# Kernel tuning notes

Hardware: AMD Instinct MI355X
Metric: run time of the kernel (lower is better)

## Reference

```python
import jax, jax.numpy as jnp
import numpy as np

N, T, D, H = 8, 1024, 128, 8

def setup_inputs() -> dict:
    key = jax.random.key(0)
    ks = jax.random.split(key, 6)
    x = jax.random.normal(ks[0], (N, T, D), dtype=jnp.float32)
    attention_mask = jax.random.randint(ks[1], (N, 1, 1, T), 0, 2).astype(jnp.bool_)
    attention_weights = jax.random.uniform(ks[2], (N, H, T, T), dtype=jnp.float32)
    # Linear(dim -> heads*dim) weights, torch convention: W @ x^T + b, W: [H*D, D]
    s = 1.0 / np.sqrt(D)
    Wq = jax.random.normal(ks[3], (H * D, D), dtype=jnp.float32) * s
    Wk = jax.random.normal(ks[4], (H * D, D), dtype=jnp.float32) * s
    Wv = jax.random.normal(ks[5], (H * D, D), dtype=jnp.float32) * s
    bq = jnp.zeros((H * D,), jnp.float32)
    bk = jnp.zeros((H * D,), jnp.float32)
    bv = jnp.zeros((H * D,), jnp.float32)
    return {"x": x, "attention_mask": attention_mask, "attention_weights": attention_weights,
            "Wq": Wq, "bq": bq, "Wk": Wk, "bk": bk, "Wv": Wv, "bv": bv}

def reference(x, attention_mask, attention_weights, Wq, bq, Wk, bk, Wv, bv):
    n, t, d = x.shape
    h = Wq.shape[0] // d
    # projections: [N,T,H*D] -> [N,H,T,D]
    q = (x @ Wq.T + bq).reshape(n, t, h, d).transpose(0, 2, 1, 3)
    k = (x @ Wk.T + bk).reshape(n, t, h, d).transpose(0, 2, 1, 3)
    v = (x @ Wv.T + bv).reshape(n, t, h, d).transpose(0, 2, 1, 3)
    # scores [N,H,T,T]
    att = jnp.einsum('nhtd,nhsd->nhts', q, k) / np.sqrt(d).astype(np.float32)
    att = att * attention_weights
    att = jnp.where(attention_mask, -jnp.inf, att)
    att = jax.nn.softmax(att, axis=-1)
    out = jnp.einsum('nhts,nhsd->nhtd', att, v)
    out = out.transpose(0, 2, 1, 3).reshape(n, t, h * d)
    out_agg = jnp.mean(out, axis=1)
    return out, jax.lax.stop_gradient(out_agg), jax.lax.stop_gradient(att)
```

## Files before the change

kernel.cpp:

```cpp
#include <hip/hip_runtime.h>
#include <hip/hip_bf16.h>
#include <hip/hip_fp16.h>

#define NB 8
#define TT 1024
#define DD 128
#define HH 8

using short8  = __attribute__((ext_vector_type(8))) short;
using floatx4 = __attribute__((ext_vector_type(4))) float;
using half8   = __attribute__((ext_vector_type(8))) _Float16;

__device__ __forceinline__ unsigned short f2bf_u(float f) {
    union { float f; unsigned u; } v; v.f = f;
    return (unsigned short)((v.u + 0x7fffu + ((v.u >> 16) & 1u)) >> 16);
}

__global__ __launch_bounds__(256, 2) void proj_kernel(
    const float* __restrict__ x,
    const float* __restrict__ Wq, const float* __restrict__ bq,
    const float* __restrict__ Wk, const float* __restrict__ bk,
    const float* __restrict__ Wv, const float* __restrict__ bv,
    unsigned short* __restrict__ qb, unsigned short* __restrict__ kb,
    unsigned short* __restrict__ vt)
{
    int b     = blockIdx.x;
    int which = b >> 10;
    int rem   = b & 1023;
    int mblk  = rem >> 3;
    int nblk  = rem & 7;
    int tid   = threadIdx.x;
    int wid   = tid >> 6, lane = tid & 63;
    int l15   = lane & 15, quad = lane >> 4;
    int m0    = mblk * 64 + wid * 16;

    const float* W    = (which == 0) ? Wq : (which == 1) ? Wk : Wv;
    const float* bias = (which == 0) ? bq : (which == 1) ? bk : bv;
    unsigned short* dst = (which == 0) ? qb : (which == 1) ? kb : vt;

    short8 a[4];
    const float* xr = x + (size_t)(m0 + l15) * DD + quad * 8;
    #pragma unroll
    for (int kk = 0; kk < 4; ++kk) {
        const float* p = xr + kk * 32;
        short8 t;
        #pragma unroll
        for (int j = 0; j < 8; ++j) t[j] = (short)f2bf_u(p[j]);
        a[kk] = t;
    }

    floatx4 acc[8];
    #pragma unroll
    for (int ct = 0; ct < 8; ++ct) acc[ct] = (floatx4){0.f, 0.f, 0.f, 0.f};

    for (int ct = 0; ct < 8; ++ct) {
        int c = nblk * 128 + ct * 16 + l15;
        const float* wr = W + (size_t)c * DD + quad * 8;
        #pragma unroll
        for (int kk = 0; kk < 4; ++kk) {
            const float* p = wr + kk * 32;
            short8 bf;
            #pragma unroll
            for (int j = 0; j < 8; ++j) bf[j] = (short)f2bf_u(p[j]);
            acc[ct] = __builtin_amdgcn_mfma_f32_16x16x32_bf16(a[kk], bf, acc[ct], 0, 0, 0);
        }
    }

    #pragma unroll
    for (int ct = 0; ct < 8; ++ct) {
        int c  = nblk * 128 + ct * 16 + l15;
        int h  = c >> 7, dd = c & 127;
        float bsv = bias[c];
        #pragma unroll
        for (int r = 0; r < 4; ++r) {
            int m = m0 + quad * 4 + r;
            int n = m >> 10, t = m & 1023;
            unsigned short v = f2bf_u(acc[ct][r] + bsv);
            size_t idx;
            if (which == 2) idx = ((size_t)(n * HH + h) * DD + dd) * TT + t;
            else            idx = ((size_t)(n * HH + h) * TT + t) * DD + dd;
            dst[idx] = v;
        }
    }
}

#define SSTRIDE 1032

__global__ __launch_bounds__(256, 2) void attn_kernel(
    const unsigned short* __restrict__ qb, const unsigned short* __restrict__ kb,
    const unsigned short* __restrict__ vt,
    const float* __restrict__ wts, const int* __restrict__ mask,
    float* __restrict__ out, float* __restrict__ outagg, float* __restrict__ att)
{
    extern __shared__ char smem[];
    _Float16* S   = (_Float16*)smem;
    float* rowinv = (float*)(smem + 32 * SSTRIDE * 2);

    int b    = blockIdx.x;
    int slot = b & 7, j = b >> 3;
    int tile = j & 31, gq = j >> 5;
    int g    = gq * 8 + slot;
    int n    = g >> 3, h = g & 7;
    int t0   = tile * 32;

    int tid = threadIdx.x;
    int wid = tid >> 6, lane = tid & 63;
    int l15 = lane & 15, quad = lane >> 4;

    const unsigned short* qp = qb + ((size_t)g * TT + t0) * DD;
    const unsigned short* kp = kb + (size_t)g * TT * DD;
    const unsigned short* vp = vt + (size_t)g * DD * TT;
    const float* wp = wts + (size_t)g * TT * TT + (size_t)t0 * TT;
    const int*   mp = mask + n * TT;
    float* attp = att + (size_t)g * TT * TT + (size_t)t0 * TT;

    short8 aq[2][4];
    #pragma unroll
    for (int rt = 0; rt < 2; ++rt)
        #pragma unroll
        for (int kk = 0; kk < 4; ++kk)
            aq[rt][kk] = *(const short8*)(qp + (size_t)(rt * 16 + l15) * DD + kk * 32 + quad * 8);

    const int c0 = wid * 256;
    const float scale = 0.08838834764831845f;
    for (int ct = 0; ct < 16; ++ct) {
        int scol = c0 + ct * 16;
        int mk = mp[scol + l15];
        float w0[4], w1[4];
        #pragma unroll
        for (int r = 0; r < 4; ++r) {
            int row = quad * 4 + r;
            w0[r] = wp[(size_t)row * TT + scol + l15];
            w1[r] = wp[(size_t)(row + 16) * TT + scol + l15];
        }
        floatx4 acc0 = {0.f,0.f,0.f,0.f}, acc1 = {0.f,0.f,0.f,0.f};
        #pragma unroll
        for (int kk = 0; kk < 4; ++kk) {
            short8 bf = *(const short8*)(kp + (size_t)(scol + l15) * DD + kk * 32 + quad * 8);
            acc0 = __builtin_amdgcn_mfma_f32_16x16x32_bf16(aq[0][kk], bf, acc0, 0, 0, 0);
            acc1 = __builtin_amdgcn_mfma_f32_16x16x32_bf16(aq[1][kk], bf, acc1, 0, 0, 0);
        }
        #pragma unroll
        for (int r = 0; r < 4; ++r) {
            int row = quad * 4 + r;
            float s0 = mk ? -65504.f : acc0[r] * scale * w0[r];
            float s1 = mk ? -65504.f : acc1[r] * scale * w1[r];
            S[row * SSTRIDE + scol + l15]        = (_Float16)s0;
            S[(row + 16) * SSTRIDE + scol + l15] = (_Float16)s1;
        }
    }
    __syncthreads();

    int row = tid >> 3;
    int jj  = tid & 7;
    _Float16* Srow = S + row * SSTRIDE + jj * 8;

    float mx = -3.0e38f;
    #pragma unroll 4
    for (int i = 0; i < 16; ++i) {
        half8 hv = *(const half8*)(Srow + i * 64);
        #pragma unroll
        for (int e = 0; e < 8; ++e) mx = fmaxf(mx, (float)hv[e]);
    }
    mx = fmaxf(mx, __shfl_xor(mx, 1));
    mx = fmaxf(mx, __shfl_xor(mx, 2));
    mx = fmaxf(mx, __shfl_xor(mx, 4));

    float sum = 0.f;
    #pragma unroll 4
    for (int i = 0; i < 16; ++i) {
        half8 hv = *(const half8*)(Srow + i * 64);
        #pragma unroll
        for (int e = 0; e < 8; ++e) sum += __expf((float)hv[e] - mx);
    }
    sum += __shfl_xor(sum, 1);
    sum += __shfl_xor(sum, 2);
    sum += __shfl_xor(sum, 4);
    float iv = 1.f / sum;
    if (jj == 0) rowinv[row] = iv;

    float* arow = attp + (size_t)row * TT + jj * 8;
    #pragma unroll 2
    for (int i = 0; i < 16; ++i) {
        half8 hv = *(const half8*)(Srow + i * 64);
        half8 ev;
        floatx4 o0, o1;
        #pragma unroll
        for (int e = 0; e < 8; ++e) {
            float ex = __expf((float)hv[e] - mx);
            ev[e] = __builtin_bit_cast(_Float16, f2bf_u(ex));
            float a = ex * iv;
            if (e < 4) o0[e] = a; else o1[e - 4] = a;
        }
        *(half8*)(Srow + i * 64) = ev;
        *(floatx4*)(arow + i * 64)     = o0;
        *(floatx4*)(arow + i * 64 + 4) = o1;
    }
    __syncthreads();

    int c0p = wid * 32;
    floatx4 o00 = {0.f,0.f,0.f,0.f}, o01 = o00, o10 = o00, o11 = o00;
    #pragma unroll 2
    for (int ks = 0; ks < 32; ++ks) {
        short8 a0 = __builtin_bit_cast(short8,
            *(const half8*)(S + (size_t)l15 * SSTRIDE + ks * 32 + quad * 8));
        short8 a1 = __builtin_bit_cast(short8,
            *(const half8*)(S + (size_t)(16 + l15) * SSTRIDE + ks * 32 + quad * 8));
        short8 b0 = *(const short8*)(vp + (size_t)(c0p + l15) * TT + ks * 32 + quad * 8);
        short8 b1 = *(const short8*)(vp + (size_t)(c0p + 16 + l15) * TT + ks * 32 + quad * 8);
        o00 = __builtin_amdgcn_mfma_f32_16x16x32_bf16(a0, b0, o00, 0, 0, 0);
        o01 = __builtin_amdgcn_mfma_f32_16x16x32_bf16(a0, b1, o01, 0, 0, 0);
        o10 = __builtin_amdgcn_mfma_f32_16x16x32_bf16(a1, b0, o10, 0, 0, 0);
        o11 = __builtin_amdgcn_mfma_f32_16x16x32_bf16(a1, b1, o11, 0, 0, 0);
    }

    #pragma unroll
    for (int ct = 0; ct < 2; ++ct) {
        int col = c0p + ct * 16 + l15;
        float agg = 0.f;
        #pragma unroll
        for (int rt = 0; rt < 2; ++rt) {
            floatx4 oo = (rt == 0) ? (ct == 0 ? o00 : o01) : (ct == 0 ? o10 : o11);
            #pragma unroll
            for (int r = 0; r < 4; ++r) {
                int rw = rt * 16 + quad * 4 + r;
                float val = oo[r] * rowinv[rw];
                out[((size_t)(n * TT + t0 + rw)) * (HH * DD) + h * DD + col] = val;
                agg += val;
            }
        }
        atomicAdd(outagg + n * (HH * DD) + h * DD + col, agg * (1.f / (float)TT));
    }
}

extern "C" void kernel_launch(void* const* d_in, const int* in_sizes, int n_in,
                              void* d_out, int out_size, void* d_ws, size_t ws_size,
                              hipStream_t stream) {
    const float* x    = (const float*)d_in[0];
    const int*   mask = (const int*)d_in[1];
    const float* wts  = (const float*)d_in[2];
    const float* Wq = (const float*)d_in[3];
    const float* bq = (const float*)d_in[4];
    const float* Wk = (const float*)d_in[5];
    const float* bk = (const float*)d_in[6];
    const float* Wv = (const float*)d_in[7];
    const float* bv = (const float*)d_in[8];

    float* out    = (float*)d_out;
    float* outagg = out + (size_t)NB * TT * HH * DD;
    float* att    = outagg + NB * HH * DD;

    unsigned short* qb = (unsigned short*)d_ws;
    unsigned short* kb = qb + (size_t)NB * HH * TT * DD;
    unsigned short* vt = kb + (size_t)NB * HH * TT * DD;

    hipMemsetAsync(outagg, 0, (size_t)NB * HH * DD * sizeof(float), stream);
    proj_kernel<<<3072, 256, 0, stream>>>(x, Wq, bq, Wk, bk, Wv, bv, qb, kb, vt);
    attn_kernel<<<2048, 256, 32 * SSTRIDE * 2 + 128, stream>>>(
        qb, kb, vt, wts, mask, out, outagg, att);
}
```

Measured before the change: 770.8 us.

## Prefetch K/weights/V tiles, transpose MFMA output for vector stores, cache softmax rows in registers

Swaps MFMA operand order so each lane owns four consecutive score columns, enabling vectorized float4 weight/mask loads and half4 LDS stores. K, weight and mask tiles are software-prefetched one or two iterations ahead, and the PV loop double-buffers V and P fragments. Softmax keeps the row slice in registers instead of re-reading LDS three times, and att/out writes use nontemporal stores. Register pressure rises, which may hurt occupancy under the 2-block launch bound.

Result: faster. 738.0 us (-4.2%).

```diff
diff --git a/kernel.cpp b/kernel.cpp
--- a/kernel.cpp
+++ b/kernel.cpp
@@ -10,6 +10,8 @@
 using short8  = __attribute__((ext_vector_type(8))) short;
 using floatx4 = __attribute__((ext_vector_type(4))) float;
 using half8   = __attribute__((ext_vector_type(8))) _Float16;
+using half4   = __attribute__((ext_vector_type(4))) _Float16;
+using intx4   = __attribute__((ext_vector_type(4))) int;
 
 __device__ __forceinline__ unsigned short f2bf_u(float f) {
     union { float f; unsigned u; } v; v.f = f;
@@ -123,31 +125,59 @@
 
     const int c0 = wid * 256;
     const float scale = 0.08838834764831845f;
+
+    const float* wrow0 = wp + (size_t)l15 * TT + c0 + quad * 4;
+    const float* wrow1 = wrow0 + (size_t)16 * TT;
+    const unsigned short* kcol = kp + (size_t)(c0 + l15) * DD + quad * 8;
+    const int* mrow = mp + c0 + quad * 4;
+    _Float16* sst0 = S + (size_t)l15 * SSTRIDE + c0 + quad * 4;
+    _Float16* sst1 = sst0 + (size_t)16 * SSTRIDE;
+
+    floatx4 w0_c, w1_c, w0_n, w1_n;
+    intx4   mk_c, mk_n;
+    short8  kf[4];
+
+    w0_c = *(const floatx4*)(wrow0);
+    w1_c = *(const floatx4*)(wrow1);
+    mk_c = *(const intx4*)(mrow);
+    w0_n = *(const floatx4*)(wrow0 + 16);
+    w1_n = *(const floatx4*)(wrow1 + 16);
+    mk_n = *(const intx4*)(mrow + 16);
+    #pragma unroll
+    for (int kk = 0; kk < 4; ++kk)
+        kf[kk] = *(const short8*)(kcol + kk * 32);
+
     for (int ct = 0; ct < 16; ++ct) {
-        int scol = c0 + ct * 16;
-        int mk = mp[scol + l15];
-        float w0[4], w1[4];
+        int ctk = (ct + 1 < 16) ? ct + 1 : 15;
+        int ctw = (ct + 2 < 16) ? ct + 2 : 15;
+        short8 kn[4];
+        #pragma unroll
+        for (int kk = 0; kk < 4; ++kk)
+            kn[kk] = *(const short8*)(kcol + ctk * 16 * DD + kk * 32);
+        floatx4 nw0 = *(const floatx4*)(wrow0 + ctw * 16);
+        floatx4 nw1 = *(const floatx4*)(wrow1 + ctw * 16);
+        intx4   nmk = *(const intx4*)(mrow + ctw * 16);
+
+        floatx4 acc0 = {0.f,0.f,0.f,0.f}, acc1 = {0.f,0.f,0.f,0.f};
+        #pragma unroll
+        for (int kk = 0; kk < 4; ++kk) {
+            acc0 = __builtin_amdgcn_mfma_f32_16x16x32_bf16(kf[kk], aq[0][kk], acc0, 0, 0, 0);
+            acc1 = __builtin_amdgcn_mfma_f32_16x16x32_bf16(kf[kk], aq[1][kk], acc1, 0, 0, 0);
+        }
+
+        half4 h0, h1;
         #pragma unroll
         for (int r = 0; r < 4; ++r) {
-            int row = quad * 4 + r;
-            w0[r] = wp[(size_t)row * TT + scol + l15];
-            w1[r] = wp[(size_t)(row + 16) * TT + scol + l15];
-        }
-        floatx4 acc0 = {0.f,0.f,0.f,0.f}, acc1 = {0.f,0.f,0.f,0.f};
-        #pragma unroll
-        for (int kk = 0; kk < 4; ++kk) {
-            short8 bf = *(const short8*)(kp + (size_t)(scol + l15) * DD + kk * 32 + quad * 8);
-            acc0 = __builtin_amdgcn_mfma_f32_16x16x32_bf16(aq[0][kk], bf, acc0, 0, 0, 0);
-            acc1 = __builtin_amdgcn_mfma_f32_16x16x32_bf16(aq[1][kk], bf, acc1, 0, 0, 0);
-        }
-        #pragma unroll
-        for (int r = 0; r < 4; ++r) {
-            int row = quad * 4 + r;
-            float s0 = mk ? -65504.f : acc0[r] * scale * w0[r];
-            float s1 = mk ? -65504.f : acc1[r] * scale * w1[r];
-            S[row * SSTRIDE + scol + l15]        = (_Float16)s0;
-            S[(row + 16) * SSTRIDE + scol + l15] = (_Float16)s1;
-        }
+            h0[r] = (_Float16)(mk_c[r] ? -65504.f : acc0[r] * scale * w0_c[r]);
+            h1[r] = (_Float16)(mk_c[r] ? -65504.f : acc1[r] * scale * w1_c[r]);
+        }
+        *(half4*)(sst0 + ct * 16) = h0;
+        *(half4*)(sst1 + ct * 16) = h1;
+
+        #pragma unroll
+        for (int kk = 0; kk < 4; ++kk) kf[kk] = kn[kk];
+        w0_c = w0_n; w1_c = w1_n; mk_c = mk_n;
+        w0_n = nw0;  w1_n = nw1;  mk_n = nmk;
     }
     __syncthreads();
 
@@ -155,24 +185,29 @@
     int jj  = tid & 7;
     _Float16* Srow = S + row * SSTRIDE + jj * 8;
 
-    float mx = -3.0e38f;
-    #pragma unroll 4
-    for (int i = 0; i < 16; ++i) {
-        half8 hv = *(const half8*)(Srow + i * 64);
-        #pragma unroll
-        for (int e = 0; e < 8; ++e) mx = fmaxf(mx, (float)hv[e]);
-    }
+    half8 hv[16];
+    #pragma unroll
+    for (int i = 0; i < 16; ++i) hv[i] = *(const half8*)(Srow + i * 64);
+
+    float m8[8];
+    #pragma unroll
+    for (int e = 0; e < 8; ++e) m8[e] = (float)hv[0][e];
+    #pragma unroll
+    for (int i = 1; i < 16; ++i)
+        #pragma unroll
+        for (int e = 0; e < 8; ++e) m8[e] = fmaxf(m8[e], (float)hv[i][e]);
+    float mx = fmaxf(fmaxf(fmaxf(m8[0], m8[1]), fmaxf(m8[2], m8[3])),
+                     fmaxf(fmaxf(m8[4], m8[5]), fmaxf(m8[6], m8[7])));
     mx = fmaxf(mx, __shfl_xor(mx, 1));
     mx = fmaxf(mx, __shfl_xor(mx, 2));
     mx = fmaxf(mx, __shfl_xor(mx, 4));
 
-    float sum = 0.f;
-    #pragma unroll 4
-    for (int i = 0; i < 16; ++i) {
-        half8 hv = *(const half8*)(Srow + i * 64);
-        #pragma unroll
-        for (int e = 0; e < 8; ++e) sum += __expf((float)hv[e] - mx);
-    }
+    float s8[8] = {0.f,0.f,0.f,0.f,0.f,0.f,0.f,0.f};
+    #pragma unroll
+    for (int i = 0; i < 16; ++i)
+        #pragma unroll
+        for (int e = 0; e < 8; ++e) s8[e] += __expf((float)hv[i][e] - mx);
+    float sum = ((s8[0] + s8[1]) + (s8[2] + s8[3])) + ((s8[4] + s8[5]) + (s8[6] + s8[7]));
     sum += __shfl_xor(sum, 1);
     sum += __shfl_xor(sum, 2);
     sum += __shfl_xor(sum, 4);
@@ -180,38 +215,48 @@
     if (jj == 0) rowinv[row] = iv;
 
     float* arow = attp + (size_t)row * TT + jj * 8;
-    #pragma unroll 2
+    #pragma unroll
     for (int i = 0; i < 16; ++i) {
-        half8 hv = *(const half8*)(Srow + i * 64);
         half8 ev;
         floatx4 o0, o1;
         #pragma unroll
         for (int e = 0; e < 8; ++e) {
-            float ex = __expf((float)hv[e] - mx);
+            float ex = __expf((float)hv[i][e] - mx);
             ev[e] = __builtin_bit_cast(_Float16, f2bf_u(ex));
             float a = ex * iv;
             if (e < 4) o0[e] = a; else o1[e - 4] = a;
         }
         *(half8*)(Srow + i * 64) = ev;
-        *(floatx4*)(arow + i * 64)     = o0;
-        *(floatx4*)(arow + i * 64 + 4) = o1;
+        __builtin_nontemporal_store(o0, (floatx4*)(arow + i * 64));
+        __builtin_nontemporal_store(o1, (floatx4*)(arow + i * 64 + 4));
     }
     __syncthreads();
 
     int c0p = wid * 32;
+    const unsigned short* vrow0 = vp + (size_t)(c0p + l15) * TT + quad * 8;
+    const unsigned short* vrow1 = vp + (size_t)(c0p + 16 + l15) * TT + quad * 8;
+    const _Float16* sp0 = S + (size_t)l15 * SSTRIDE + quad * 8;
+    const _Float16* sp1 = S + (size_t)(16 + l15) * SSTRIDE + quad * 8;
+
     floatx4 o00 = {0.f,0.f,0.f,0.f}, o01 = o00, o10 = o00, o11 = o00;
-    #pragma unroll 2
+    short8 vb0 = *(const short8*)(vrow0);
+    short8 vb1 = *(const short8*)(vrow1);
+    short8 pa0 = __builtin_bit_cast(short8, *(const half8*)(sp0));
+    short8 pa1 = __builtin_bit_cast(short8, *(const half8*)(sp1));
+
     for (int ks = 0; ks < 32; ++ks) {
-        short8 a0 = __builtin_bit_cast(short8,
-            *(const half8*)(S + (size_t)l15 * SSTRIDE + ks * 32 + quad * 8));
-        short8 a1 = __builtin_bit_cast(short8,
-            *(const half8*)(S + (size_t)(16 + l15) * SSTRIDE + ks * 32 + quad * 8));
-        short8 b0 = *(const short8*)(vp + (size_t)(c0p + l15) * TT + ks * 32 + quad * 8);
-        short8 b1 = *(const short8*)(vp + (size_t)(c0p + 16 + l15) * TT + ks * 32 + quad * 8);
-        o00 = __builtin_amdgcn_mfma_f32_16x16x32_bf16(a0, b0, o00, 0, 0, 0);
-        o01 = __builtin_amdgcn_mfma_f32_16x16x32_bf16(a0, b1, o01, 0, 0, 0);
-        o10 = __builtin_amdgcn_mfma_f32_16x16x32_bf16(a1, b0, o10, 0, 0, 0);
-        o11 = __builtin_amdgcn_mfma_f32_16x16x32_bf16(a1, b1, o11, 0, 0, 0);
+        int ksn = (ks + 1 < 32) ? ks + 1 : 31;
+        short8 nv0 = *(const short8*)(vrow0 + ksn * 32);
+        short8 nv1 = *(const short8*)(vrow1 + ksn * 32);
+        short8 na0 = __builtin_bit_cast(short8, *(const half8*)(sp0 + ksn * 32));
+        short8 na1 = __builtin_bit_cast(short8, *(const half8*)(sp1 + ksn * 32));
+
+        o00 = __builtin_amdgcn_mfma_f32_16x16x32_bf16(pa0, vb0, o00, 0, 0, 0);
+        o01 = __builtin_amdgcn_mfma_f32_16x16x32_bf16(pa0, vb1, o01, 0, 0, 0);
+        o10 = __builtin_amdgcn_mfma_f32_16x16x32_bf16(pa1, vb0, o10, 0, 0, 0);
+        o11 = __builtin_amdgcn_mfma_f32_16x16x32_bf16(pa1, vb1, o11, 0, 0, 0);
+
+        vb0 = nv0; vb1 = nv1; pa0 = na0; pa1 = na1;
     }
 
     #pragma unroll
@@ -225,7 +270,8 @@
             for (int r = 0; r < 4; ++r) {
                 int rw = rt * 16 + quad * 4 + r;
                 float val = oo[r] * rowinv[rw];
-                out[((size_t)(n * TT + t0 + rw)) * (HH * DD) + h * DD + col] = val;
+                __builtin_nontemporal_store(
+                    val, &out[((size_t)(n * TT + t0 + rw)) * (HH * DD) + h * DD + col]);
                 agg += val;
             }
         }
```
